# Kernel tuning notes

Hardware: AMD Instinct MI355X
Metric: run time of the kernel (lower is better)

Reference implementation:

```python
import jax, jax.numpy as jnp
import numpy as np

N_NODES = 100000
N_EDGES = 1000000
D = 128  # latent_dim


def setup_inputs() -> dict:
    key = jax.random.key(0)
    ks = jax.random.split(key, 8)
    z = jax.random.normal(ks[0], (N_NODES, D), dtype=jnp.float32)
    edge_index = jax.random.randint(ks[1], (2, N_EDGES), 0, N_NODES, dtype=jnp.int64)
    # MLP params: Linear(2D->D), Linear(D->D//2), Linear(D//2->1)
    def lin(k, fan_in, fan_out):
        kw, kb = jax.random.split(k)
        bound = 1.0 / np.sqrt(fan_in)
        W = jax.random.uniform(kw, (fan_in, fan_out), jnp.float32, -bound, bound)
        b = jax.random.uniform(kb, (fan_out,), jnp.float32, -bound, bound)
        return W, b
    W1, b1 = lin(ks[2], 2 * D, D)
    W2, b2 = lin(ks[3], D, D // 2)
    W3, b3 = lin(ks[4], D // 2, 1)
    return {"z": z, "edge_index": edge_index, "W1": W1, "b1": b1,
            "W2": W2, "b2": b2, "W3": W3, "b3": b3}


def reference(z, edge_index, W1, b1, W2, b2, W3, b3):
    # Gather src/dst node embeddings and concat: [E, 2D]
    h = jnp.concatenate([z[edge_index[0]], z[edge_index[1]]], axis=-1)
    h = jax.nn.relu(h @ W1 + b1)      # [E, D]
    h = jax.nn.relu(h @ W2 + b2)      # [E, D//2]
    out = h @ W3 + b3                 # [E, 1]
    return out  # sigmoid=False default
```

## Files before the change

### kernel.cpp

```cpp
#include <hip/hip_runtime.h>
#include <hip/hip_bf16.h>

#define NE 1000000
#define NN 100000
#define NWT 31250
#define NGT 6250

typedef __attribute__((ext_vector_type(8))) short bf16x8;
typedef __attribute__((ext_vector_type(4))) float f32x4;

__device__ __forceinline__ unsigned short f2bf(float f) {
  unsigned u = __builtin_bit_cast(unsigned, f);
  u += 0x7fffu + ((u >> 16) & 1u);
  return (unsigned short)(u >> 16);
}
__device__ __forceinline__ float bf2f(unsigned short s) {
  return __builtin_bit_cast(float, (unsigned)s << 16);
}

__global__ void prep(const float* __restrict__ W1, const float* __restrict__ W2,
                     unsigned short* __restrict__ afw, unsigned short* __restrict__ fw2) {
  int tid = blockIdx.x * 256 + threadIdx.x;
  if (tid < 32768) {
    int j = tid & 7, l = (tid >> 3) & 63, kb = (tid >> 9) & 3, mt = tid >> 11;
    int k = kb * 32 + (l >> 4) * 8 + j;
    int n = mt * 16 + (l & 15);
    float v = (n < 128) ? W1[k * 128 + n] : W1[(128 + k) * 128 + (n - 128)];
    afw[tid] = f2bf(v);
  } else if (tid < 40960) {
    int t = tid - 32768;
    int j = t & 7, l = (t >> 3) & 63, kb = (t >> 9) & 3, nt = t >> 11;
    fw2[t] = f2bf(W2[(kb * 32 + (l >> 4) * 8 + j) * 64 + nt * 16 + (l & 15)]);
  }
}

__global__ __launch_bounds__(256, 4) void node_gemm(
    const float* __restrict__ z, const unsigned short* __restrict__ afw,
    const float* __restrict__ b1, unsigned short* __restrict__ h1ab) {
  const int l = threadIdx.x & 63, w = threadIdx.x >> 6;
  const int wtile = blockIdx.x * 4 + w;
  if (wtile >= NGT) return;
  const int c = l & 15, g = l >> 4;
  const int node0 = wtile * 16;

  f32x4 acc[16] = {};
#pragma unroll
  for (int kb = 0; kb < 4; kb++) {
    const float* zp = z + (node0 + c) * 128 + kb * 32 + g * 8;
    float4 z0 = *(const float4*)zp;
    float4 z1 = *(const float4*)(zp + 4);
    bf16x8 bfrag;
    bfrag[0] = f2bf(z0.x); bfrag[1] = f2bf(z0.y); bfrag[2] = f2bf(z0.z); bfrag[3] = f2bf(z0.w);
    bfrag[4] = f2bf(z1.x); bfrag[5] = f2bf(z1.y); bfrag[6] = f2bf(z1.z); bfrag[7] = f2bf(z1.w);
#pragma unroll
    for (int mt = 0; mt < 16; mt++) {
      bf16x8 af = *(const bf16x8*)(afw + ((mt * 4 + kb) * 64 + l) * 8);
      acc[mt] = __builtin_amdgcn_mfma_f32_16x16x32_bf16(af, bfrag, acc[mt], 0, 0, 0);
    }
  }
#pragma unroll
  for (int mt = 0; mt < 16; mt++) {
    const int f0 = mt * 16 + g * 4;
    float v0 = acc[mt][0], v1 = acc[mt][1], v2 = acc[mt][2], v3 = acc[mt][3];
    if (mt < 8) {
      float4 bb = *(const float4*)(b1 + f0);
      v0 += bb.x; v1 += bb.y; v2 += bb.z; v3 += bb.w;
    }
    unsigned lo = (unsigned)f2bf(v0) | ((unsigned)f2bf(v1) << 16);
    unsigned hi = (unsigned)f2bf(v2) | ((unsigned)f2bf(v3) << 16);
    uint2 pk = {lo, hi};
    *(uint2*)(h1ab + (node0 + c) * 256 + f0) = pk;
  }
}

__global__ __launch_bounds__(256, 5) void mlp_edge(
    const unsigned short* __restrict__ h1ab, const int* __restrict__ edge,
    const unsigned short* __restrict__ fw2,
    const float* __restrict__ b2, const float* __restrict__ W3,
    const float* __restrict__ b3, float* __restrict__ out) {
  __shared__ __align__(16) unsigned short sfw2[8192];
  {
    const int t = threadIdx.x;
#pragma unroll
    for (int it = 0; it < 4; it++)
      ((bf16x8*)sfw2)[it * 256 + t] = ((const bf16x8*)fw2)[it * 256 + t];
  }
  __syncthreads();

  const int l = threadIdx.x & 63, w = threadIdx.x >> 6;
  const int wt = blockIdx.x * 4 + w;
  if (wt >= NWT) return;
  const int c = l & 15, g = l >> 4;
  const int eBase = wt * 32;

  unsigned srcO[2], dstO[2];
#pragma unroll
  for (int mt = 0; mt < 2; mt++) {
    int e = eBase + mt * 16 + c;
    srcO[mt] = (unsigned)edge[e] * 512u;
    dstO[mt] = (unsigned)edge[NE + e] * 512u + 256u;
  }
  const char* hb = (const char*)h1ab;
  const unsigned kbase = (unsigned)g * 16u;

  f32x4 acc2[2][4] = {};
#pragma unroll
  for (int kb = 0; kb < 4; kb++) {
    const unsigned koff = (unsigned)kb * 64u + kbase;
    bf16x8 a2[2];
#pragma unroll
    for (int mt = 0; mt < 2; mt++) {
      bf16x8 ha = *(const bf16x8*)(hb + srcO[mt] + koff);
      bf16x8 hd = *(const bf16x8*)(hb + dstO[mt] + koff);
#pragma unroll
      for (int j = 0; j < 8; j++) {
        float v = bf2f((unsigned short)ha[j]) + bf2f((unsigned short)hd[j]);
        a2[mt][j] = (short)f2bf(fmaxf(v, 0.f));
      }
    }
#pragma unroll
    for (int nt = 0; nt < 4; nt++) {
      bf16x8 bf = ((const bf16x8*)sfw2)[(nt * 4 + kb) * 64 + l];
#pragma unroll
      for (int mt = 0; mt < 2; mt++)
        acc2[mt][nt] = __builtin_amdgcn_mfma_f32_16x16x32_bf16(a2[mt], bf, acc2[mt][nt], 0, 0, 0);
    }
  }

  float w3v[4], b2v[4];
#pragma unroll
  for (int nt = 0; nt < 4; nt++) {
    w3v[nt] = W3[nt * 16 + c];
    b2v[nt] = b2[nt * 16 + c];
  }
  const float bias3 = b3[0];
#pragma unroll
  for (int mt = 0; mt < 2; mt++) {
#pragma unroll
    for (int i = 0; i < 4; i++) {
      float t = 0.f;
#pragma unroll
      for (int nt = 0; nt < 4; nt++)
        t += fmaxf(acc2[mt][nt][i] + b2v[nt], 0.f) * w3v[nt];
      t += __shfl_xor(t, 1);
      t += __shfl_xor(t, 2);
      t += __shfl_xor(t, 4);
      t += __shfl_xor(t, 8);
      if (c == 0) out[eBase + mt * 16 + g * 4 + i] = t + bias3;
    }
  }
}

extern "C" void kernel_launch(void* const* d_in, const int* in_sizes, int n_in,
                              void* d_out, int out_size, void* d_ws, size_t ws_size,
                              hipStream_t stream) {
  const float* z  = (const float*)d_in[0];
  const int* edge = (const int*)d_in[1];
  const float* W1 = (const float*)d_in[2];
  const float* b1 = (const float*)d_in[3];
  const float* W2 = (const float*)d_in[4];
  const float* b2 = (const float*)d_in[5];
  const float* W3 = (const float*)d_in[6];
  const float* b3 = (const float*)d_in[7];
  float* out = (float*)d_out;

  unsigned short* afw  = (unsigned short*)d_ws;
  unsigned short* fw2  = afw + 32768;
  unsigned short* h1ab = fw2 + 8192;

  prep<<<160, 256, 0, stream>>>(W1, W2, afw, fw2);
  node_gemm<<<(NGT + 3) / 4, 256, 0, stream>>>(z, afw, b1, h1ab);
  mlp_edge<<<(NWT + 3) / 4, 256, 0, stream>>>(h1ab, edge, fw2, b2, W3, b3, out);
}
```

Before: 206.5 us.

## Stage W1 fragments in LDS, double node tile, prefetch edge gathers, use packed bf16 conversion

The node GEMM now copies the 64KB W1 fragment table into shared memory and processes 32 nodes per wave instead of 16, so each weight fragment feeds two MFMAs. All z loads are issued up front. The edge MLP loads all eight src/dst gather vectors per edge before computing, which puts more memory requests in flight. Float-to-bf16 packing goes through the hardware paired conversion intrinsic. The costs are more registers and LDS, and lower occupancy bounds (node_gemm 2, mlp_edge 4).

```diff
diff --git a/kernel.cpp b/kernel.cpp
--- a/kernel.cpp
+++ b/kernel.cpp
@@ -1,10 +1,11 @@
 #include <hip/hip_runtime.h>
 #include <hip/hip_bf16.h>
+#include <string.h>
 
 #define NE 1000000
 #define NN 100000
 #define NWT 31250
-#define NGT 6250
+#define NGT2 3125
 
 typedef __attribute__((ext_vector_type(8))) short bf16x8;
 typedef __attribute__((ext_vector_type(4))) float f32x4;
@@ -14,8 +15,17 @@
   u += 0x7fffu + ((u >> 16) & 1u);
   return (unsigned short)(u >> 16);
 }
-__device__ __forceinline__ float bf2f(unsigned short s) {
-  return __builtin_bit_cast(float, (unsigned)s << 16);
+__device__ __forceinline__ unsigned pk2(float a, float b) {
+  __hip_bfloat162 h = __float22bfloat162_rn(make_float2(a, b));
+  unsigned r;
+  memcpy(&r, &h, 4);
+  return r;
+}
+__device__ __forceinline__ float lo2f(unsigned u) {
+  return __builtin_bit_cast(float, u << 16);
+}
+__device__ __forceinline__ float hi2f(unsigned u) {
+  return __builtin_bit_cast(float, u & 0xffff0000u);
 }
 
 __global__ void prep(const float* __restrict__ W1, const float* __restrict__ W2,
@@ -34,46 +44,69 @@
   }
 }
 
-__global__ __launch_bounds__(256, 4) void node_gemm(
+__global__ __launch_bounds__(256, 2) void node_gemm(
     const float* __restrict__ z, const unsigned short* __restrict__ afw,
     const float* __restrict__ b1, unsigned short* __restrict__ h1ab) {
+  __shared__ __align__(16) bf16x8 sfw[4096];
+  {
+    const int t = threadIdx.x;
+#pragma unroll
+    for (int it = 0; it < 16; it++)
+      sfw[it * 256 + t] = ((const bf16x8*)afw)[it * 256 + t];
+  }
+  __syncthreads();
+
   const int l = threadIdx.x & 63, w = threadIdx.x >> 6;
-  const int wtile = blockIdx.x * 4 + w;
-  if (wtile >= NGT) return;
+  const int wt = blockIdx.x * 4 + w;
+  if (wt >= NGT2) return;
   const int c = l & 15, g = l >> 4;
-  const int node0 = wtile * 16;
-
-  f32x4 acc[16] = {};
+  const int n0 = wt * 32;
+
+  float4 zl[2][4][2];
+#pragma unroll
+  for (int grp = 0; grp < 2; grp++)
+#pragma unroll
+    for (int kb = 0; kb < 4; kb++) {
+      const float* zp = z + (n0 + grp * 16 + c) * 128 + kb * 32 + g * 8;
+      zl[grp][kb][0] = *(const float4*)zp;
+      zl[grp][kb][1] = *(const float4*)(zp + 4);
+    }
+
+  f32x4 acc[2][16] = {};
 #pragma unroll
   for (int kb = 0; kb < 4; kb++) {
-    const float* zp = z + (node0 + c) * 128 + kb * 32 + g * 8;
-    float4 z0 = *(const float4*)zp;
-    float4 z1 = *(const float4*)(zp + 4);
-    bf16x8 bfrag;
-    bfrag[0] = f2bf(z0.x); bfrag[1] = f2bf(z0.y); bfrag[2] = f2bf(z0.z); bfrag[3] = f2bf(z0.w);
-    bfrag[4] = f2bf(z1.x); bfrag[5] = f2bf(z1.y); bfrag[6] = f2bf(z1.z); bfrag[7] = f2bf(z1.w);
+    bf16x8 bfrag[2];
+#pragma unroll
+    for (int grp = 0; grp < 2; grp++) {
+      float4 a = zl[grp][kb][0], b = zl[grp][kb][1];
+      uint4 u = {pk2(a.x, a.y), pk2(a.z, a.w), pk2(b.x, b.y), pk2(b.z, b.w)};
+      bfrag[grp] = __builtin_bit_cast(bf16x8, u);
+    }
 #pragma unroll
     for (int mt = 0; mt < 16; mt++) {
-      bf16x8 af = *(const bf16x8*)(afw + ((mt * 4 + kb) * 64 + l) * 8);
-      acc[mt] = __builtin_amdgcn_mfma_f32_16x16x32_bf16(af, bfrag, acc[mt], 0, 0, 0);
-    }
-  }
-#pragma unroll
-  for (int mt = 0; mt < 16; mt++) {
-    const int f0 = mt * 16 + g * 4;
-    float v0 = acc[mt][0], v1 = acc[mt][1], v2 = acc[mt][2], v3 = acc[mt][3];
-    if (mt < 8) {
-      float4 bb = *(const float4*)(b1 + f0);
-      v0 += bb.x; v1 += bb.y; v2 += bb.z; v3 += bb.w;
-    }
-    unsigned lo = (unsigned)f2bf(v0) | ((unsigned)f2bf(v1) << 16);
-    unsigned hi = (unsigned)f2bf(v2) | ((unsigned)f2bf(v3) << 16);
-    uint2 pk = {lo, hi};
-    *(uint2*)(h1ab + (node0 + c) * 256 + f0) = pk;
-  }
-}
-
-__global__ __launch_bounds__(256, 5) void mlp_edge(
+      bf16x8 af = sfw[(mt * 4 + kb) * 64 + l];
+      acc[0][mt] = __builtin_amdgcn_mfma_f32_16x16x32_bf16(af, bfrag[0], acc[0][mt], 0, 0, 0);
+      acc[1][mt] = __builtin_amdgcn_mfma_f32_16x16x32_bf16(af, bfrag[1], acc[1][mt], 0, 0, 0);
+    }
+  }
+
+#pragma unroll
+  for (int grp = 0; grp < 2; grp++)
+#pragma unroll
+    for (int mt = 0; mt < 16; mt++) {
+      const int f0 = mt * 16 + g * 4;
+      float v0 = acc[grp][mt][0], v1 = acc[grp][mt][1];
+      float v2 = acc[grp][mt][2], v3 = acc[grp][mt][3];
+      if (mt < 8) {
+        float4 bb = *(const float4*)(b1 + f0);
+        v0 += bb.x; v1 += bb.y; v2 += bb.z; v3 += bb.w;
+      }
+      uint2 pk = {pk2(v0, v1), pk2(v2, v3)};
+      *(uint2*)(h1ab + (n0 + grp * 16 + c) * 256 + f0) = pk;
+    }
+}
+
+__global__ __launch_bounds__(256, 4) void mlp_edge(
     const unsigned short* __restrict__ h1ab, const int* __restrict__ edge,
     const unsigned short* __restrict__ fw2,
     const float* __restrict__ b2, const float* __restrict__ W3,
@@ -93,30 +126,35 @@
   const int c = l & 15, g = l >> 4;
   const int eBase = wt * 32;
 
-  unsigned srcO[2], dstO[2];
+  const char* hb = (const char*)h1ab;
+  const unsigned kbase = (unsigned)g * 16u;
+
+  uint4 sv[2][4], dv[2][4];
 #pragma unroll
   for (int mt = 0; mt < 2; mt++) {
     int e = eBase + mt * 16 + c;
-    srcO[mt] = (unsigned)edge[e] * 512u;
-    dstO[mt] = (unsigned)edge[NE + e] * 512u + 256u;
-  }
-  const char* hb = (const char*)h1ab;
-  const unsigned kbase = (unsigned)g * 16u;
+    unsigned so = (unsigned)edge[e] * 512u + kbase;
+    unsigned dofs = (unsigned)edge[NE + e] * 512u + 256u + kbase;
+#pragma unroll
+    for (int kb = 0; kb < 4; kb++) {
+      sv[mt][kb] = *(const uint4*)(hb + so + kb * 64u);
+      dv[mt][kb] = *(const uint4*)(hb + dofs + kb * 64u);
+    }
+  }
 
   f32x4 acc2[2][4] = {};
 #pragma unroll
   for (int kb = 0; kb < 4; kb++) {
-    const unsigned koff = (unsigned)kb * 64u + kbase;
     bf16x8 a2[2];
 #pragma unroll
     for (int mt = 0; mt < 2; mt++) {
-      bf16x8 ha = *(const bf16x8*)(hb + srcO[mt] + koff);
-      bf16x8 hd = *(const bf16x8*)(hb + dstO[mt] + koff);
-#pragma unroll
-      for (int j = 0; j < 8; j++) {
-        float v = bf2f((unsigned short)ha[j]) + bf2f((unsigned short)hd[j]);
-        a2[mt][j] = (short)f2bf(fmaxf(v, 0.f));
-      }
+      uint4 s = sv[mt][kb], d = dv[mt][kb];
+      uint4 r;
+      r.x = pk2(fmaxf(lo2f(s.x) + lo2f(d.x), 0.f), fmaxf(hi2f(s.x) + hi2f(d.x), 0.f));
+      r.y = pk2(fmaxf(lo2f(s.y) + lo2f(d.y), 0.f), fmaxf(hi2f(s.y) + hi2f(d.y), 0.f));
+      r.z = pk2(fmaxf(lo2f(s.z) + lo2f(d.z), 0.f), fmaxf(hi2f(s.z) + hi2f(d.z), 0.f));
+      r.w = pk2(fmaxf(lo2f(s.w) + lo2f(d.w), 0.f), fmaxf(hi2f(s.w) + hi2f(d.w), 0.f));
+      a2[mt] = __builtin_bit_cast(bf16x8, r);
     }
 #pragma unroll
     for (int nt = 0; nt < 4; nt++) {
@@ -169,6 +207,6 @@
   unsigned short* h1ab = fw2 + 8192;
 
   prep<<<160, 256, 0, stream>>>(W1, W2, afw, fw2);
-  node_gemm<<<(NGT + 3) / 4, 256, 0, stream>>>(z, afw, b1, h1ab);
+  node_gemm<<<(NGT2 + 3) / 4, 256, 0, stream>>>(z, afw, b1, h1ab);
   mlp_edge<<<(NWT + 3) / 4, 256, 0, stream>>>(h1ab, edge, fw2, b2, W3, b3, out);
 }
```

After: 204.8 us. No clear change (-0.8%).
